# Optimization experiments

Measured on AMD Instinct MI355X. Metric: run time of the kernel, lower is better.

Reference implementation:

```python
import jax, jax.numpy as jnp
import numpy as np

B, H, S, D = 4, 16, 2048, 64
NEG = -9e15


def setup_inputs() -> dict:
    key = jax.random.key(0)
    kq, kk, kv = jax.random.split(key, 3)
    q = jax.random.normal(kq, (B, H, S, D), dtype=jnp.float32)
    k = jax.random.normal(kk, (B, H, S, D), dtype=jnp.float32)
    v = jax.random.normal(kv, (B, H, S, D), dtype=jnp.float32)
    # causal mask: 1 where attention allowed, 0 where masked
    mask = jnp.tril(jnp.ones((S, S), dtype=jnp.int32))[None, None]
    return {"q": q, "k": k, "v": v, "mask": mask}


def reference(q, k, v, mask):
    d_k = q.shape[-1]
    # [B,H,S,S] scores
    scores = jnp.einsum("bhqd,bhkd->bhqk", q, k) / jnp.sqrt(jnp.float32(d_k))
    scores = jnp.where(mask == 0, jnp.float32(NEG), scores)
    attn = jax.nn.softmax(scores, axis=-1)
    return jnp.einsum("bhqk,bhkd->bhqd", attn, v)
```

## Files before the change

kernel.cpp:

```cpp
#include <hip/hip_runtime.h>

#define SLEN 2048
#define DH 64
#define NH 64
#define KVB 64
#define NT 32
#define NP 16
#define NEGBIG (-1e30f)
#define SCALE 0.18033688011112042f

typedef __attribute__((ext_vector_type(8))) short bf16x8;
typedef __attribute__((ext_vector_type(8))) unsigned short u16x8;
typedef __attribute__((ext_vector_type(16))) float f32x16;
typedef __attribute__((ext_vector_type(4))) float f32x4;
typedef __attribute__((ext_vector_type(4))) unsigned int u32x4;

__device__ __forceinline__ ushort f2bf(float f) {
  union { float f; unsigned int u; } v; v.f = f;
  unsigned int r = v.u + 0x7fffu + ((v.u >> 16) & 1u);
  return (ushort)(r >> 16);
}

__device__ __forceinline__ unsigned int cvtpk(float lo, float hi2) {
  unsigned int r;
  asm("v_cvt_pk_bf16_f32 %0, %1, %2" : "=v"(r) : "v"(lo), "v"(hi2));
  return r;
}

__device__ __forceinline__ float xsumh(float x) { return x + __shfl_xor(x, 32); }

__device__ __forceinline__ void gload16(const ushort* g, ushort* l) {
  __builtin_amdgcn_global_load_lds(
      (const __attribute__((address_space(1))) void*)g,
      (__attribute__((address_space(3))) void*)l, 16, 0, 0);
}

__global__ __launch_bounds__(256) void prep_k(const float* __restrict__ Kg,
                                              ushort* __restrict__ wsK) {
  const int head = blockIdx.x, tile = blockIdx.y, tid = threadIdx.x;
  const float* src = Kg + ((size_t)head * SLEN + (size_t)tile * KVB) * DH;
  ushort* dst = wsK + ((size_t)head * NT + tile) * (KVB * DH);
#pragma unroll
  for (int i = 0; i < 2; ++i) {
    const int id = tid + i * 256;
    const int r = id >> 3, c = id & 7;
    float4 a = *reinterpret_cast<const float4*>(src + r * DH + c * 8);
    float4 b = *reinterpret_cast<const float4*>(src + r * DH + c * 8 + 4);
    u16x8 t;
    t[0] = f2bf(a.x); t[1] = f2bf(a.y); t[2] = f2bf(a.z); t[3] = f2bf(a.w);
    t[4] = f2bf(b.x); t[5] = f2bf(b.y); t[6] = f2bf(b.z); t[7] = f2bf(b.w);
    *reinterpret_cast<u16x8*>(dst + r * DH + ((c ^ (r & 7)) * 8)) = t;
  }
}

__global__ __launch_bounds__(256) void prep_v(const float* __restrict__ Vg,
                                              ushort* __restrict__ wsV) {
  __shared__ float Vl[KVB][DH + 1];
  const int head = blockIdx.x, tile = blockIdx.y, tid = threadIdx.x;
  const float* src = Vg + ((size_t)head * SLEN + (size_t)tile * KVB) * DH;
#pragma unroll
  for (int i = 0; i < 4; ++i) {
    const int n = tid + i * 256;
    const int row = n >> 4, c4 = (n & 15) << 2;
    *reinterpret_cast<float4*>(&Vl[row][c4]) =
        *reinterpret_cast<const float4*>(src + row * DH + c4);
  }
  __syncthreads();
  ushort* dst = wsV + ((size_t)head * NT + tile) * (KVB * DH);
#pragma unroll
  for (int i = 0; i < 2; ++i) {
    const int id = tid + i * 256;
    const int d = id >> 3, c = id & 7;
    u16x8 t;
#pragma unroll
    for (int j = 0; j < 8; ++j) t[j] = f2bf(Vl[c * 8 + j][d]);
    *reinterpret_cast<u16x8*>(dst + d * DH + ((c ^ (d & 7)) * 8)) = t;
  }
}

__device__ __forceinline__ void qkt(const ushort* __restrict__ Kl,
                                    const bf16x8* qf, f32x16& s0, f32x16& s1,
                                    int ql, int hi) {
  s0 = (f32x16)0.0f; s1 = (f32x16)0.0f;
  __builtin_amdgcn_s_setprio(1);
#pragma unroll
  for (int ks = 0; ks < 4; ++ks) {
    const int c = ((ks * 2 + hi) ^ (ql & 7)) * 8;
    bf16x8 kf0 = *reinterpret_cast<const bf16x8*>(Kl + ql * 64 + c);
    bf16x8 kf1 = *reinterpret_cast<const bf16x8*>(Kl + (32 + ql) * 64 + c);
    s0 = __builtin_amdgcn_mfma_f32_32x32x16_bf16(kf0, qf[ks], s0, 0, 0, 0);
    s1 = __builtin_amdgcn_mfma_f32_32x32x16_bf16(kf1, qf[ks], s1, 0, 0, 0);
  }
  __builtin_amdgcn_s_setprio(0);
}

__device__ __forceinline__ void fin(const ushort* __restrict__ Vl,
                                    f32x16& s0, f32x16& s1, f32x16& o0,
                                    f32x16& o1, f32x4& lv, int t,
                                    int tl, int q0, int ql, int hi) {
  if (t == tl) {
    const int qg = q0 + ql;
#pragma unroll
    for (int r = 0; r < 16; ++r) {
      const int kr = t * 64 + (r & 3) + 8 * (r >> 2) + 4 * hi;
      if (kr > qg)      s0[r] = NEGBIG;
      if (kr + 32 > qg) s1[r] = NEGBIG;
    }
  }

#pragma unroll
  for (int r = 0; r < 16; ++r) s0[r] = __builtin_exp2f(s0[r]);
#pragma unroll
  for (int r = 0; r < 16; ++r) s1[r] = __builtin_exp2f(s1[r]);

#pragma unroll
  for (int r = 0; r < 16; ++r) lv[r & 3] += s0[r] + s1[r];

  unsigned int pw0[8], pw1[8];
#pragma unroll
  for (int g = 0; g < 4; ++g)
#pragma unroll
    for (int j = 0; j < 2; ++j) {
      pw0[g * 2 + j] = cvtpk(s0[4 * g + 2 * j], s0[4 * g + 2 * j + 1]);
      pw1[g * 2 + j] = cvtpk(s1[4 * g + 2 * j], s1[4 * g + 2 * j + 1]);
    }

  __builtin_amdgcn_s_setprio(1);
#pragma unroll
  for (int st = 0; st < 4; ++st) {
    const unsigned int* PW = (st < 2) ? pw0 : pw1;
    const int KH = st & 1;
    const unsigned int a0 = PW[4 * KH + 0], a1 = PW[4 * KH + 1];
    const unsigned int b0 = PW[4 * KH + 2], b1 = PW[4 * KH + 3];
    const unsigned int s0w = hi ? a0 : b0, s1w = hi ? a1 : b1;
    const unsigned int r0 = __shfl_xor(s0w, 32), r1 = __shfl_xor(s1w, 32);
    const unsigned int k0 = hi ? b0 : a0, k1 = hi ? b1 : a1;
    u32x4 fu;
    fu[0] = hi ? r0 : k0; fu[1] = hi ? r1 : k1;
    fu[2] = hi ? k0 : r0; fu[3] = hi ? k1 : r1;
    const bf16x8 pf = __builtin_bit_cast(bf16x8, fu);
    const int cv = ((st * 2 + hi) ^ (ql & 7)) * 8;
    const bf16x8 vf0 = *reinterpret_cast<const bf16x8*>(Vl + ql * 64 + cv);
    const bf16x8 vf1 = *reinterpret_cast<const bf16x8*>(Vl + (32 + ql) * 64 + cv);
    o0 = __builtin_amdgcn_mfma_f32_32x32x16_bf16(vf0, pf, o0, 0, 0, 0);
    o1 = __builtin_amdgcn_mfma_f32_32x32x16_bf16(vf1, pf, o1, 0, 0, 0);
  }
  __builtin_amdgcn_s_setprio(0);
}

__device__ __forceinline__ void load_q(const float* Qh, int q0, int ql, int hi,
                                       bf16x8* qf) {
  const float* qrow = Qh + (size_t)(q0 + ql) * DH;
#pragma unroll
  for (int ks = 0; ks < 4; ++ks) {
    const int d0 = ks * 16 + hi * 8;
    float4 a = *reinterpret_cast<const float4*>(qrow + d0);
    float4 b = *reinterpret_cast<const float4*>(qrow + d0 + 4);
    bf16x8 t;
    t[0] = (short)f2bf(a.x * SCALE); t[1] = (short)f2bf(a.y * SCALE);
    t[2] = (short)f2bf(a.z * SCALE); t[3] = (short)f2bf(a.w * SCALE);
    t[4] = (short)f2bf(b.x * SCALE); t[5] = (short)f2bf(b.y * SCALE);
    t[6] = (short)f2bf(b.z * SCALE); t[7] = (short)f2bf(b.w * SCALE);
    qf[ks] = t;
  }
}

__device__ __forceinline__ void epi(float* Ow, float* Oh, const f32x16& o,
                                    float invl, int q0, int subd, int lane) {
  const int ql = lane & 31, hi = lane >> 5;
#pragma unroll
  for (int g = 0; g < 4; ++g) {
    float4 vv = make_float4(o[4 * g] * invl, o[4 * g + 1] * invl,
                            o[4 * g + 2] * invl, o[4 * g + 3] * invl);
    *reinterpret_cast<float4*>(Ow + ql * 36 + 8 * g + 4 * hi) = vv;
  }
#pragma unroll
  for (int i = 0; i < 4; ++i) {
    const int qr = (lane >> 3) + i * 8;
    const int c4 = (lane & 7) * 4;
    float4 vv = *reinterpret_cast<const float4*>(Ow + qr * 36 + c4);
    *reinterpret_cast<float4*>(Oh + (size_t)(q0 + qr) * DH + subd * 32 + c4) = vv;
  }
}

__global__ __launch_bounds__(128, 2) void attn_fwd7(
    const float* __restrict__ Qg, const ushort* __restrict__ wsK,
    const ushort* __restrict__ wsV, float* __restrict__ Og) {
  __shared__ __align__(16) float smem[8192];
  ushort* stg = (ushort*)smem;

  const int head = blockIdx.x;
  const int p    = blockIdx.y;
  const int tid  = threadIdx.x;
  const int w    = tid >> 6;
  const int lane = tid & 63;
  const int hi   = lane >> 5;
  const int ql   = lane & 31;

  const int q0A = p * 64 + w * 32;
  const int q0B = (31 - p) * 64 + w * 32;
  const int tlA = p;
  const int tlB = 31 - p;
  const int nt  = 32 - p;

  const float*  Qh    = Qg + (size_t)head * SLEN * DH;
  float*        Oh    = Og + (size_t)head * SLEN * DH;
  const ushort* kbase = wsK + (size_t)head * (NT * KVB * DH);
  const ushort* vbase = wsV + (size_t)head * (NT * KVB * DH);

#define STAGE(buf, t)                                                          \
  do {                                                                         \
    const size_t tb_ = (size_t)(t) * 4096;                                     \
    _Pragma("unroll")                                                          \
    for (int j_ = 0; j_ < 4; ++j_) {                                           \
      gload16(kbase + tb_ + j_ * 1024 + tid * 8,                               \
              stg + (buf) * 8192 + j_ * 1024 + tid * 8);                       \
      gload16(vbase + tb_ + j_ * 1024 + tid * 8,                               \
              stg + (buf) * 8192 + 4096 + j_ * 1024 + tid * 8);                \
    }                                                                          \
  } while (0)

  STAGE(0, 0);

  bf16x8 qfA[4], qfB[4];
  load_q(Qh, q0A, ql, hi, qfA);
  load_q(Qh, q0B, ql, hi, qfB);

  f32x16 oA0 = (f32x16)0.0f, oA1 = (f32x16)0.0f;
  f32x16 oB0 = (f32x16)0.0f, oB1 = (f32x16)0.0f;
  f32x4 lvA = (f32x4)0.0f, lvB = (f32x4)0.0f;

  __syncthreads();

  int cur = 0;
  for (int t = 0; t < nt; ++t) {
    if (t + 1 < nt) STAGE(cur ^ 1, t + 1);

    const ushort* Kl = stg + cur * 8192;
    const ushort* Vl = Kl + 4096;
    const bool doA = (t <= tlA);

    f32x16 sB0, sB1, sA0, sA1;
    qkt(Kl, qfB, sB0, sB1, ql, hi);
    if (doA) qkt(Kl, qfA, sA0, sA1, ql, hi);
    fin(Vl, sB0, sB1, oB0, oB1, lvB, t, tlB, q0B, ql, hi);
    if (doA) fin(Vl, sA0, sA1, oA0, oA1, lvA, t, tlA, q0A, ql, hi);

    __syncthreads();
    cur ^= 1;
  }
#undef STAGE

  const float lAs = xsumh(lvA[0] + lvA[1] + lvA[2] + lvA[3]);
  const float lBs = xsumh(lvB[0] + lvB[1] + lvB[2] + lvB[3]);

  float* Ow = smem + w * 1152;
  const float iA = 1.0f / lAs, iB = 1.0f / lBs;
  epi(Ow, Oh, oA0, iA, q0A, 0, lane);
  epi(Ow, Oh, oA1, iA, q0A, 1, lane);
  epi(Ow, Oh, oB0, iB, q0B, 0, lane);
  epi(Ow, Oh, oB1, iB, q0B, 1, lane);
}

extern "C" void kernel_launch(void* const* d_in, const int* in_sizes, int n_in,
                              void* d_out, int out_size, void* d_ws, size_t ws_size,
                              hipStream_t stream) {
  const float* q = (const float*)d_in[0];
  const float* k = (const float*)d_in[1];
  const float* v = (const float*)d_in[2];
  float* out = (float*)d_out;

  const size_t per = (size_t)NH * SLEN * DH;
  ushort* wsK = (ushort*)d_ws;
  ushort* wsV = wsK + per;

  prep_k<<<dim3(NH, NT), 256, 0, stream>>>(k, wsK);
  prep_v<<<dim3(NH, NT), 256, 0, stream>>>(v, wsV);
  attn_fwd7<<<dim3(NH, NP), 128, 0, stream>>>(q, wsK, wsV, out);
}
```

Before: 91.61 us.

## Triple-buffer K/V tiles with vmcnt waits and fuse K/V prep kernels

The attention kernel moves from double to triple buffering of K/V tiles in LDS, prefetching two tiles ahead. It replaces __syncthreads with explicit s_waitcnt vmcnt plus s_barrier so loads for the tile after next stay in flight across the barrier. The separate K and V bf16 conversion kernels are merged into one launch, which removes a kernel launch. LDS use grows from 32KB to 48KB per block, which could reduce occupancy, and the hand-written vmcnt counts must match the number of outstanding loads.

Measured after the change: 118.1 us. +28.9%, slower.

```diff
diff --git a/kernel.cpp b/kernel.cpp
--- a/kernel.cpp
+++ b/kernel.cpp
@@ -35,46 +35,44 @@
       (__attribute__((address_space(3))) void*)l, 16, 0, 0);
 }
 
-__global__ __launch_bounds__(256) void prep_k(const float* __restrict__ Kg,
-                                              ushort* __restrict__ wsK) {
+__global__ __launch_bounds__(256) void prep_kv(const float* __restrict__ Kg,
+                                               const float* __restrict__ Vg,
+                                               ushort* __restrict__ wsK,
+                                               ushort* __restrict__ wsV) {
+  __shared__ float Vsh[KVB][DH + 1];
   const int head = blockIdx.x, tile = blockIdx.y, tid = threadIdx.x;
-  const float* src = Kg + ((size_t)head * SLEN + (size_t)tile * KVB) * DH;
-  ushort* dst = wsK + ((size_t)head * NT + tile) * (KVB * DH);
+  const size_t goff = ((size_t)head * SLEN + (size_t)tile * KVB) * DH;
+  const float* srcK = Kg + goff;
+  const float* srcV = Vg + goff;
+  ushort* dstK = wsK + ((size_t)head * NT + tile) * (KVB * DH);
+  ushort* dstV = wsV + ((size_t)head * NT + tile) * (KVB * DH);
 #pragma unroll
   for (int i = 0; i < 2; ++i) {
     const int id = tid + i * 256;
     const int r = id >> 3, c = id & 7;
-    float4 a = *reinterpret_cast<const float4*>(src + r * DH + c * 8);
-    float4 b = *reinterpret_cast<const float4*>(src + r * DH + c * 8 + 4);
+    float4 a = *reinterpret_cast<const float4*>(srcK + r * DH + c * 8);
+    float4 b = *reinterpret_cast<const float4*>(srcK + r * DH + c * 8 + 4);
     u16x8 t;
     t[0] = f2bf(a.x); t[1] = f2bf(a.y); t[2] = f2bf(a.z); t[3] = f2bf(a.w);
     t[4] = f2bf(b.x); t[5] = f2bf(b.y); t[6] = f2bf(b.z); t[7] = f2bf(b.w);
-    *reinterpret_cast<u16x8*>(dst + r * DH + ((c ^ (r & 7)) * 8)) = t;
-  }
-}
-
-__global__ __launch_bounds__(256) void prep_v(const float* __restrict__ Vg,
-                                              ushort* __restrict__ wsV) {
-  __shared__ float Vl[KVB][DH + 1];
-  const int head = blockIdx.x, tile = blockIdx.y, tid = threadIdx.x;
-  const float* src = Vg + ((size_t)head * SLEN + (size_t)tile * KVB) * DH;
+    *reinterpret_cast<u16x8*>(dstK + r * DH + ((c ^ (r & 7)) * 8)) = t;
+  }
 #pragma unroll
   for (int i = 0; i < 4; ++i) {
     const int n = tid + i * 256;
     const int row = n >> 4, c4 = (n & 15) << 2;
-    *reinterpret_cast<float4*>(&Vl[row][c4]) =
-        *reinterpret_cast<const float4*>(src + row * DH + c4);
+    *reinterpret_cast<float4*>(&Vsh[row][c4]) =
+        *reinterpret_cast<const float4*>(srcV + row * DH + c4);
   }
   __syncthreads();
-  ushort* dst = wsV + ((size_t)head * NT + tile) * (KVB * DH);
 #pragma unroll
   for (int i = 0; i < 2; ++i) {
     const int id = tid + i * 256;
     const int d = id >> 3, c = id & 7;
     u16x8 t;
 #pragma unroll
-    for (int j = 0; j < 8; ++j) t[j] = f2bf(Vl[c * 8 + j][d]);
-    *reinterpret_cast<u16x8*>(dst + d * DH + ((c ^ (d & 7)) * 8)) = t;
+    for (int j = 0; j < 8; ++j) t[j] = f2bf(Vsh[c * 8 + j][d]);
+    *reinterpret_cast<u16x8*>(dstV + d * DH + ((c ^ (d & 7)) * 8)) = t;
   }
 }
 
@@ -107,12 +105,10 @@
       if (kr + 32 > qg) s1[r] = NEGBIG;
     }
   }
-
 #pragma unroll
   for (int r = 0; r < 16; ++r) s0[r] = __builtin_exp2f(s0[r]);
 #pragma unroll
   for (int r = 0; r < 16; ++r) s1[r] = __builtin_exp2f(s1[r]);
-
 #pragma unroll
   for (int r = 0; r < 16; ++r) lv[r & 3] += s0[r] + s1[r];
 
@@ -183,10 +179,10 @@
   }
 }
 
-__global__ __launch_bounds__(128, 2) void attn_fwd7(
+__global__ __launch_bounds__(128, 2) void attn_fwd14(
     const float* __restrict__ Qg, const ushort* __restrict__ wsK,
     const ushort* __restrict__ wsV, float* __restrict__ Og) {
-  __shared__ __align__(16) float smem[8192];
+  __shared__ __align__(16) float smem[12288];
   ushort* stg = (ushort*)smem;
 
   const int head = blockIdx.x;
@@ -221,6 +217,7 @@
   } while (0)
 
   STAGE(0, 0);
+  STAGE(1, 1);
 
   bf16x8 qfA[4], qfB[4];
   load_q(Qh, q0A, ql, hi, qfA);
@@ -230,11 +227,17 @@
   f32x16 oB0 = (f32x16)0.0f, oB1 = (f32x16)0.0f;
   f32x4 lvA = (f32x4)0.0f, lvB = (f32x4)0.0f;
 
-  __syncthreads();
+  asm volatile("s_waitcnt vmcnt(8)" ::: "memory");
+  __builtin_amdgcn_s_barrier();
+  __builtin_amdgcn_sched_barrier(0);
 
   int cur = 0;
   for (int t = 0; t < nt; ++t) {
-    if (t + 1 < nt) STAGE(cur ^ 1, t + 1);
+    const bool pre = (t + 2 < nt);
+    if (pre) {
+      int nb = cur + 2; if (nb >= 3) nb -= 3;
+      STAGE(nb, t + 2);
+    }
 
     const ushort* Kl = stg + cur * 8192;
     const ushort* Vl = Kl + 4096;
@@ -246,8 +249,15 @@
     fin(Vl, sB0, sB1, oB0, oB1, lvB, t, tlB, q0B, ql, hi);
     if (doA) fin(Vl, sA0, sA1, oA0, oA1, lvA, t, tlA, q0A, ql, hi);
 
-    __syncthreads();
-    cur ^= 1;
+    if (pre) {
+      asm volatile("s_waitcnt vmcnt(8)" ::: "memory");
+    } else {
+      asm volatile("s_waitcnt vmcnt(0)" ::: "memory");
+    }
+    __builtin_amdgcn_s_barrier();
+    __builtin_amdgcn_sched_barrier(0);
+
+    ++cur; if (cur >= 3) cur = 0;
   }
 #undef STAGE
 
@@ -274,7 +284,6 @@
   ushort* wsK = (ushort*)d_ws;
   ushort* wsV = wsK + per;
 
-  prep_k<<<dim3(NH, NT), 256, 0, stream>>>(k, wsK);
-  prep_v<<<dim3(NH, NT), 256, 0, stream>>>(v, wsV);
-  attn_fwd7<<<dim3(NH, NP), 128, 0, stream>>>(q, wsK, wsV, out);
-}
+  prep_kv<<<dim3(NH, NT), 256, 0, stream>>>(k, v, wsK, wsV);
+  attn_fwd14<<<dim3(NH, NP), 128, 0, stream>>>(q, wsK, wsV, out);
+}
```
